# Optimization experiments

Hardware: AMD Instinct MI355X
Metric: run time of the kernel (lower is better)

The kernel has to match this reference:

```python
import jax, jax.numpy as jnp
import numpy as np

N_NODES = 100000
N_EDGES = 1600000


def _gcn_conv(x, src, dst, W, b, n_nodes):
    """PyG GCNConv: add self-loops, symmetric norm, linear, scatter-add."""
    h = x @ W  # [N, out]
    # append self-loops
    loop = jnp.arange(n_nodes, dtype=src.dtype)
    s = jnp.concatenate([src, loop])
    d = jnp.concatenate([dst, loop])
    # degree over destinations (with self-loops)
    deg = jax.ops.segment_sum(jnp.ones_like(d, dtype=h.dtype), d, num_segments=n_nodes)
    dinv = jax.lax.rsqrt(jnp.maximum(deg, 1.0))
    norm = dinv[s] * dinv[d]  # [E+N]
    msg = h[s] * norm[:, None]  # [E+N, out] gather + scale
    out = jax.ops.segment_sum(msg, d, num_segments=n_nodes)  # scatter-add
    return out + b


def setup_inputs() -> dict:
    key = jax.random.key(0)
    k1, k2, k3, k4 = jax.random.split(key, 4)
    x = jax.random.normal(k1, (N_NODES, 10), dtype=jnp.float32)
    edge_index = jax.random.randint(k2, (2, N_EDGES), 0, N_NODES, dtype=jnp.int64)
    W1 = jax.random.normal(k3, (10, 64), dtype=jnp.float32) * (1.0 / np.sqrt(10))
    b1 = jnp.zeros((64,), dtype=jnp.float32)
    W2 = jax.random.normal(k4, (64, 10), dtype=jnp.float32) * (1.0 / np.sqrt(64))
    b2 = jnp.zeros((10,), dtype=jnp.float32)
    return {"x": x, "edge_index": edge_index, "W1": W1, "b1": b1, "W2": W2, "b2": b2}


def reference(x, edge_index, W1, b1, W2, b2):
    src, dst = edge_index[0], edge_index[1]
    h = _gcn_conv(x, src, dst, W1, b1, N_NODES)
    h = jax.nn.relu(h)
    # dropout is identity in eval mode
    h = _gcn_conv(h, src, dst, W2, b2, N_NODES)
    return jax.nn.log_softmax(h, axis=1)
```

## Files before the change

### kernel.cpp

```cpp
#include <hip/hip_runtime.h>
#include <hip/hip_fp16.h>

#define N_NODES 100000
#define N_EDGES 1600000

#define NPB   256
#define NB    391
#define ABLK  256
#define ATHR  1024
#define BSLOT 64
#define CAP   64

typedef unsigned int u32;

__device__ __forceinline__ float2 h2f2(u32 u) {
    __half2 h = *reinterpret_cast<__half2*>(&u);
    return __half22float2(h);
}

__global__ __launch_bounds__(ATHR) void bucket_kernel(
    const int* __restrict__ src, const int* __restrict__ dst,
    int* __restrict__ gcnt, int* __restrict__ pairs, int E) {
    __shared__ int lcnt[NB];
    const int tid = threadIdx.x, blk = blockIdx.x;
    for (int b = tid; b < NB; b += ATHR) lcnt[b] = 0;
    __syncthreads();

    const int chunk = (E + gridDim.x - 1) / gridDim.x;
    const int e0 = blk * chunk;
    const int e1 = min(e0 + chunk, E);

    for (int e = e0 + tid; e < e1; e += ATHR) {
        int d = dst[e];
        int b = d >> 8;
        int p = (src[e] << 8) | (d & 255);
        int pos = atomicAdd(&lcnt[b], 1);
        if (pos < BSLOT) pairs[(size_t)b * (ABLK * BSLOT) + blk * BSLOT + pos] = p;
    }
    __syncthreads();
    for (int b = tid; b < NB; b += ATHR)
        gcnt[b * ABLK + blk] = min(lcnt[b], BSLOT);
}

__global__ __launch_bounds__(1024) void csr_kernel(
    const int* __restrict__ gcnt, const int* __restrict__ pairs,
    const float* __restrict__ x, int* __restrict__ cnt, int* __restrict__ slist,
    float* __restrict__ dinv, u32* __restrict__ xh, u32* __restrict__ th, int N) {
    __shared__ int ofs[NPB];
    __shared__ int gc[ABLK];
    const int b = blockIdx.x, tid = threadIdx.x;
    if (tid < NPB) ofs[tid] = 0;
    if (tid < ABLK) gc[tid] = gcnt[b * ABLK + tid];
    __syncthreads();
    const int* pb = pairs + (size_t)b * (ABLK * BSLOT);
    const int node0 = b * NPB;
    for (int i = tid; i < ABLK * BSLOT; i += 1024) {
        int r = i >> 6;
        int j = i & 63;
        if (j < gc[r]) {
            int p = pb[i];
            int dl = p & 255;
            int pos = atomicAdd(&ofs[dl], 1);
            if (pos < CAP) slist[(size_t)(node0 + dl) * CAP + pos] = p >> 8;
        }
    }
    __syncthreads();
    if (tid < NPB) {
        int node = node0 + tid;
        if (node < N) {
            int deg = min(ofs[tid], CAP);
            cnt[node] = deg;
            int padded = (deg + 3) & ~3;
            for (int j = deg; j < padded; ++j) slist[(size_t)node * CAP + j] = N_NODES;
            float di = rsqrtf((float)deg + 1.0f);
            dinv[node] = di;
            u32 h[8];
#pragma unroll
            for (int k = 0; k < 5; ++k) {
                __half2 hh = __floats2half2_rn(x[(size_t)node * 10 + 2 * k] * di,
                                               x[(size_t)node * 10 + 2 * k + 1] * di);
                h[k] = *reinterpret_cast<u32*>(&hh);
            }
            h[5] = h[6] = h[7] = 0u;
            u32* row = xh + (size_t)node * 8;
            ((uint4*)row)[0] = make_uint4(h[0], h[1], h[2], h[3]);
            ((uint4*)row)[1] = make_uint4(h[4], h[5], h[6], h[7]);
        }
    }
    if (b == 0 && tid == 0) {
        u32* rx = xh + (size_t)N * 8;
        u32* rt = th + (size_t)N * 8;
        ((uint4*)rx)[0] = make_uint4(0, 0, 0, 0); ((uint4*)rx)[1] = make_uint4(0, 0, 0, 0);
        ((uint4*)rt)[0] = make_uint4(0, 0, 0, 0); ((uint4*)rt)[1] = make_uint4(0, 0, 0, 0);
    }
}

__global__ void aggmlp_kernel(const u32* __restrict__ vh, const int* __restrict__ cnt,
                              const int* __restrict__ slist, const float* __restrict__ dinv,
                              const float* __restrict__ W1, const float* __restrict__ b1,
                              const float* __restrict__ W2, u32* __restrict__ th, int N) {
    __shared__ float sW1[640];
    __shared__ float sW2[640];
    __shared__ float sb1[64];
    for (int k = threadIdx.x; k < 640; k += blockDim.x) { sW1[k] = W1[k]; sW2[k] = W2[k]; }
    if (threadIdx.x < 64) sb1[threadIdx.x] = b1[threadIdx.x];
    __syncthreads();
    int gt = blockIdx.x * blockDim.x + threadIdx.x;
    int i = gt >> 1, cg = gt & 1;
    if (i >= N) return;
    int degi = cnt[i];
    const int* lst = slist + (size_t)i * CAP;
    float a[8];
    {
        uint4 s = *(((const uint4*)(vh + (size_t)i * 8)) + cg);
        float2 f0 = h2f2(s.x), f1 = h2f2(s.y), f2 = h2f2(s.z), f3 = h2f2(s.w);
        a[0] = f0.x; a[1] = f0.y; a[2] = f1.x; a[3] = f1.y;
        a[4] = f2.x; a[5] = f2.y; a[6] = f3.x; a[7] = f3.y;
    }
    for (int k = 0; k < degi; k += 4) {
        int4 s4 = *reinterpret_cast<const int4*>(lst + k);
        uint4 q0 = *(((const uint4*)(vh + (size_t)s4.x * 8)) + cg);
        uint4 q1 = *(((const uint4*)(vh + (size_t)s4.y * 8)) + cg);
        uint4 q2 = *(((const uint4*)(vh + (size_t)s4.z * 8)) + cg);
        uint4 q3 = *(((const uint4*)(vh + (size_t)s4.w * 8)) + cg);
        float2 f;
        f = h2f2(q0.x); a[0] += f.x; a[1] += f.y;  f = h2f2(q0.y); a[2] += f.x; a[3] += f.y;
        f = h2f2(q0.z); a[4] += f.x; a[5] += f.y;  f = h2f2(q0.w); a[6] += f.x; a[7] += f.y;
        f = h2f2(q1.x); a[0] += f.x; a[1] += f.y;  f = h2f2(q1.y); a[2] += f.x; a[3] += f.y;
        f = h2f2(q1.z); a[4] += f.x; a[5] += f.y;  f = h2f2(q1.w); a[6] += f.x; a[7] += f.y;
        f = h2f2(q2.x); a[0] += f.x; a[1] += f.y;  f = h2f2(q2.y); a[2] += f.x; a[3] += f.y;
        f = h2f2(q2.z); a[4] += f.x; a[5] += f.y;  f = h2f2(q2.w); a[6] += f.x; a[7] += f.y;
        f = h2f2(q3.x); a[0] += f.x; a[1] += f.y;  f = h2f2(q3.y); a[2] += f.x; a[3] += f.y;
        f = h2f2(q3.z); a[4] += f.x; a[5] += f.y;  f = h2f2(q3.w); a[6] += f.x; a[7] += f.y;
    }
    float t0 = __shfl_xor(a[0], 1), t1 = __shfl_xor(a[1], 1);
    float t2 = __shfl_xor(a[2], 1), t3 = __shfl_xor(a[3], 1);
    float t4 = __shfl_xor(a[4], 1), t5 = __shfl_xor(a[5], 1);
    float t6 = __shfl_xor(a[6], 1), t7 = __shfl_xor(a[7], 1);
    float di = dinv[i];
    float ax[10];
    if (cg == 0) {
        ax[0]=a[0]; ax[1]=a[1]; ax[2]=a[2]; ax[3]=a[3]; ax[4]=a[4];
        ax[5]=a[5]; ax[6]=a[6]; ax[7]=a[7]; ax[8]=t0;   ax[9]=t1;
    } else {
        ax[0]=t0; ax[1]=t1; ax[2]=t2; ax[3]=t3; ax[4]=t4;
        ax[5]=t5; ax[6]=t6; ax[7]=t7; ax[8]=a[0]; ax[9]=a[1];
    }
#pragma unroll
    for (int k = 0; k < 10; ++k) ax[k] *= di;
    float o[10];
#pragma unroll
    for (int k = 0; k < 10; ++k) o[k] = 0.f;
    const int c0 = cg * 32;
    for (int c = c0; c < c0 + 32; ++c) {
        float y = sb1[c];
#pragma unroll
        for (int k = 0; k < 10; ++k) y = fmaf(ax[k], sW1[k * 64 + c], y);
        y = fmaxf(y, 0.f);
#pragma unroll
        for (int k = 0; k < 10; ++k) o[k] = fmaf(y, sW2[c * 10 + k], o[k]);
    }
#pragma unroll
    for (int k = 0; k < 10; ++k) o[k] += __shfl_xor(o[k], 1);
#pragma unroll
    for (int k = 0; k < 10; ++k) o[k] *= di;
    u32* row = th + (size_t)i * 8;
    if (cg == 0) {
        __half2 h0 = __floats2half2_rn(o[0], o[1]);
        __half2 h1 = __floats2half2_rn(o[2], o[3]);
        __half2 h2 = __floats2half2_rn(o[4], o[5]);
        __half2 h3 = __floats2half2_rn(o[6], o[7]);
        ((uint4*)row)[0] = make_uint4(*reinterpret_cast<u32*>(&h0), *reinterpret_cast<u32*>(&h1),
                                      *reinterpret_cast<u32*>(&h2), *reinterpret_cast<u32*>(&h3));
    } else {
        __half2 h4 = __floats2half2_rn(o[8], o[9]);
        ((uint4*)row)[1] = make_uint4(*reinterpret_cast<u32*>(&h4), 0u, 0u, 0u);
    }
}

__global__ void aggout_kernel(const u32* __restrict__ vh, const int* __restrict__ cnt,
                              const int* __restrict__ slist, const float* __restrict__ dinv,
                              const float* __restrict__ b2, float* __restrict__ out, int N) {
    int gt = blockIdx.x * blockDim.x + threadIdx.x;
    int i = gt >> 1, cg = gt & 1;
    bool valid = (i < N);
    float a[8];
#pragma unroll
    for (int k = 0; k < 8; ++k) a[k] = 0.f;
    if (valid) {
        int degi = cnt[i];
        const int* lst = slist + (size_t)i * CAP;
        {
            uint4 s = *(((const uint4*)(vh + (size_t)i * 8)) + cg);
            float2 f0 = h2f2(s.x), f1 = h2f2(s.y), f2 = h2f2(s.z), f3 = h2f2(s.w);
            a[0] = f0.x; a[1] = f0.y; a[2] = f1.x; a[3] = f1.y;
            a[4] = f2.x; a[5] = f2.y; a[6] = f3.x; a[7] = f3.y;
        }
        for (int k = 0; k < degi; k += 4) {
            int4 s4 = *reinterpret_cast<const int4*>(lst + k);
            uint4 q0 = *(((const uint4*)(vh + (size_t)s4.x * 8)) + cg);
            uint4 q1 = *(((const uint4*)(vh + (size_t)s4.y * 8)) + cg);
            uint4 q2 = *(((const uint4*)(vh + (size_t)s4.z * 8)) + cg);
            uint4 q3 = *(((const uint4*)(vh + (size_t)s4.w * 8)) + cg);
            float2 f;
            f = h2f2(q0.x); a[0] += f.x; a[1] += f.y;  f = h2f2(q0.y); a[2] += f.x; a[3] += f.y;
            f = h2f2(q0.z); a[4] += f.x; a[5] += f.y;  f = h2f2(q0.w); a[6] += f.x; a[7] += f.y;
            f = h2f2(q1.x); a[0] += f.x; a[1] += f.y;  f = h2f2(q1.y); a[2] += f.x; a[3] += f.y;
            f = h2f2(q1.z); a[4] += f.x; a[5] += f.y;  f = h2f2(q1.w); a[6] += f.x; a[7] += f.y;
            f = h2f2(q2.x); a[0] += f.x; a[1] += f.y;  f = h2f2(q2.y); a[2] += f.x; a[3] += f.y;
            f = h2f2(q2.z); a[4] += f.x; a[5] += f.y;  f = h2f2(q2.w); a[6] += f.x; a[7] += f.y;
            f = h2f2(q3.x); a[0] += f.x; a[1] += f.y;  f = h2f2(q3.y); a[2] += f.x; a[3] += f.y;
            f = h2f2(q3.z); a[4] += f.x; a[5] += f.y;  f = h2f2(q3.w); a[6] += f.x; a[7] += f.y;
        }
    }
    float v8 = __shfl_xor(a[0], 1);
    float v9 = __shfl_xor(a[1], 1);
    if (valid && cg == 0) {
        float di = dinv[i];
        float v[10] = { a[0], a[1], a[2], a[3], a[4], a[5], a[6], a[7], v8, v9 };
        float m = -1e30f;
#pragma unroll
        for (int c = 0; c < 10; ++c) {
            v[c] = fmaf(di, v[c], b2[c]);
            m = fmaxf(m, v[c]);
        }
        float s = 0.f;
#pragma unroll
        for (int c = 0; c < 10; ++c) s += __expf(v[c] - m);
        float lse = __logf(s) + m;
        float2* po = (float2*)(out + (size_t)i * 10);
#pragma unroll
        for (int c = 0; c < 5; ++c) po[c] = make_float2(v[2 * c] - lse, v[2 * c + 1] - lse);
    }
}

extern "C" void kernel_launch(void* const* d_in, const int* in_sizes, int n_in,
                              void* d_out, int out_size, void* d_ws, size_t ws_size,
                              hipStream_t stream) {
    const float* x  = (const float*)d_in[0];
    const int*   ei = (const int*)d_in[1];
    const float* W1 = (const float*)d_in[2];
    const float* b1 = (const float*)d_in[3];
    const float* W2 = (const float*)d_in[4];
    const float* b2 = (const float*)d_in[5];
    float* out = (float*)d_out;

    const int N = N_NODES, E = N_EDGES;
    const int* src = ei;
    const int* dst = ei + E;

    int*   gcnt  = (int*)d_ws;
    int*   pairs = gcnt + (size_t)NB * ABLK;
    int*   cnt   = pairs + (size_t)NB * ABLK * BSLOT;
    int*   slist = cnt + N;
    float* dinv  = (float*)(slist + (size_t)N * CAP);
    u32*   xh    = (u32*)(dinv + N);
    u32*   th    = xh + (size_t)(N + 1) * 8;

    bucket_kernel<<<ABLK, ATHR, 0, stream>>>(src, dst, gcnt, pairs, E);
    csr_kernel<<<NB, 1024, 0, stream>>>(gcnt, pairs, x, cnt, slist, dinv, xh, th, N);
    aggmlp_kernel<<<(2 * N + 255) / 256, 256, 0, stream>>>(xh, cnt, slist, dinv, W1, b1, W2, th, N);
    aggout_kernel<<<(2 * N + 255) / 256, 256, 0, stream>>>(th, cnt, slist, dinv, b2, out, N);
}
```

Measured before the change: 83.17 us.

## Fuse the four GCN kernels into one persistent kernel with grid barriers

Merges bucketing, CSR build, layer-1 aggregation plus MLP, and layer-2 aggregation plus log-softmax into a single persistent kernel of 256 blocks of 1024 threads. The stages are separated by atomic spin-wait grid barriers, and a tiny init kernel resets the barrier counter. The aim is to remove the inter-kernel launch gaps and drain/fill between stages. In exchange the grid size and occupancy are fixed for every phase: 391 buckets are processed by 256 blocks, leaving some blocks with two. Correctness also depends on all blocks being co-resident.

New measurement: 174.3 us. 2.1x slower.

```diff
diff --git a/kernel.cpp b/kernel.cpp
--- a/kernel.cpp
+++ b/kernel.cpp
@@ -6,8 +6,8 @@
 
 #define NPB   256
 #define NB    391
-#define ABLK  256
-#define ATHR  1024
+#define GBLK  256
+#define GTHR  1024
 #define BSLOT 64
 #define CAP   64
 
@@ -18,219 +18,239 @@
     return __half22float2(h);
 }
 
-__global__ __launch_bounds__(ATHR) void bucket_kernel(
+__global__ void init_kernel(int* __restrict__ bar) {
+    if (threadIdx.x == 0) *bar = 0;
+}
+
+__device__ __forceinline__ void gridbar(int* bar, int target) {
+    __syncthreads();
+    if (threadIdx.x == 0) {
+        __threadfence();
+        atomicAdd(bar, 1);
+        while (__hip_atomic_load(bar, __ATOMIC_RELAXED, __HIP_MEMORY_SCOPE_AGENT) < target) {
+            __builtin_amdgcn_s_sleep(1);
+        }
+        __threadfence();
+    }
+    __syncthreads();
+}
+
+__global__ __launch_bounds__(GTHR) void mega_kernel(
     const int* __restrict__ src, const int* __restrict__ dst,
-    int* __restrict__ gcnt, int* __restrict__ pairs, int E) {
-    __shared__ int lcnt[NB];
-    const int tid = threadIdx.x, blk = blockIdx.x;
-    for (int b = tid; b < NB; b += ATHR) lcnt[b] = 0;
-    __syncthreads();
-
-    const int chunk = (E + gridDim.x - 1) / gridDim.x;
-    const int e0 = blk * chunk;
-    const int e1 = min(e0 + chunk, E);
-
-    for (int e = e0 + tid; e < e1; e += ATHR) {
-        int d = dst[e];
-        int b = d >> 8;
-        int p = (src[e] << 8) | (d & 255);
-        int pos = atomicAdd(&lcnt[b], 1);
-        if (pos < BSLOT) pairs[(size_t)b * (ABLK * BSLOT) + blk * BSLOT + pos] = p;
-    }
-    __syncthreads();
-    for (int b = tid; b < NB; b += ATHR)
-        gcnt[b * ABLK + blk] = min(lcnt[b], BSLOT);
-}
-
-__global__ __launch_bounds__(1024) void csr_kernel(
-    const int* __restrict__ gcnt, const int* __restrict__ pairs,
-    const float* __restrict__ x, int* __restrict__ cnt, int* __restrict__ slist,
-    float* __restrict__ dinv, u32* __restrict__ xh, u32* __restrict__ th, int N) {
-    __shared__ int ofs[NPB];
-    __shared__ int gc[ABLK];
-    const int b = blockIdx.x, tid = threadIdx.x;
-    if (tid < NPB) ofs[tid] = 0;
-    if (tid < ABLK) gc[tid] = gcnt[b * ABLK + tid];
-    __syncthreads();
-    const int* pb = pairs + (size_t)b * (ABLK * BSLOT);
-    const int node0 = b * NPB;
-    for (int i = tid; i < ABLK * BSLOT; i += 1024) {
-        int r = i >> 6;
-        int j = i & 63;
-        if (j < gc[r]) {
-            int p = pb[i];
-            int dl = p & 255;
-            int pos = atomicAdd(&ofs[dl], 1);
-            if (pos < CAP) slist[(size_t)(node0 + dl) * CAP + pos] = p >> 8;
-        }
-    }
-    __syncthreads();
-    if (tid < NPB) {
-        int node = node0 + tid;
-        if (node < N) {
-            int deg = min(ofs[tid], CAP);
-            cnt[node] = deg;
-            int padded = (deg + 3) & ~3;
-            for (int j = deg; j < padded; ++j) slist[(size_t)node * CAP + j] = N_NODES;
-            float di = rsqrtf((float)deg + 1.0f);
-            dinv[node] = di;
-            u32 h[8];
-#pragma unroll
-            for (int k = 0; k < 5; ++k) {
-                __half2 hh = __floats2half2_rn(x[(size_t)node * 10 + 2 * k] * di,
-                                               x[(size_t)node * 10 + 2 * k + 1] * di);
-                h[k] = *reinterpret_cast<u32*>(&hh);
-            }
-            h[5] = h[6] = h[7] = 0u;
-            u32* row = xh + (size_t)node * 8;
-            ((uint4*)row)[0] = make_uint4(h[0], h[1], h[2], h[3]);
-            ((uint4*)row)[1] = make_uint4(h[4], h[5], h[6], h[7]);
-        }
-    }
-    if (b == 0 && tid == 0) {
+    const float* __restrict__ x,
+    const float* __restrict__ W1, const float* __restrict__ b1,
+    const float* __restrict__ W2, const float* __restrict__ b2,
+    int* __restrict__ bar, int* __restrict__ gcnt, int* __restrict__ pairs,
+    int* __restrict__ cnt, int* __restrict__ slist, float* __restrict__ dinv,
+    u32* __restrict__ xh, u32* __restrict__ th, float* __restrict__ out,
+    int N, int E) {
+
+    __shared__ int   lcnt[NB];
+    __shared__ int   s_ofs[NPB];
+    __shared__ int   s_gc[GBLK];
+    __shared__ float sW1[640];
+    __shared__ float sW2[640];
+    __shared__ float sb1[64];
+
+    const int tid = threadIdx.x;
+    const int blk = blockIdx.x;
+
+    for (int b = tid; b < NB; b += GTHR) lcnt[b] = 0;
+    __syncthreads();
+    {
+        const int chunk = (E + GBLK - 1) / GBLK;
+        const int e0 = blk * chunk;
+        const int e1 = min(e0 + chunk, E);
+        for (int e = e0 + tid; e < e1; e += GTHR) {
+            int d = dst[e];
+            int b = d >> 8;
+            int p = (src[e] << 8) | (d & 255);
+            int pos = atomicAdd(&lcnt[b], 1);
+            if (pos < BSLOT) pairs[(size_t)b * (GBLK * BSLOT) + blk * BSLOT + pos] = p;
+        }
+        __syncthreads();
+        for (int b = tid; b < NB; b += GTHR)
+            gcnt[b * GBLK + blk] = min(lcnt[b], BSLOT);
+    }
+    gridbar(bar, GBLK);
+
+    for (int b = blk; b < NB; b += GBLK) {
+        if (tid < NPB) s_ofs[tid] = 0;
+        if (tid < GBLK) s_gc[tid] = gcnt[b * GBLK + tid];
+        __syncthreads();
+        const int* pb = pairs + (size_t)b * (GBLK * BSLOT);
+        const int node0 = b * NPB;
+        for (int i = tid; i < GBLK * BSLOT; i += GTHR) {
+            int r = i >> 6;
+            int j = i & 63;
+            if (j < s_gc[r]) {
+                int p = pb[i];
+                int dl = p & 255;
+                int pos = atomicAdd(&s_ofs[dl], 1);
+                if (pos < CAP) slist[(size_t)(node0 + dl) * CAP + pos] = p >> 8;
+            }
+        }
+        __syncthreads();
+        if (tid < NPB) {
+            int node = node0 + tid;
+            if (node < N) {
+                int deg = min(s_ofs[tid], CAP);
+                cnt[node] = deg;
+                int padded = (deg + 3) & ~3;
+                for (int j = deg; j < padded; ++j) slist[(size_t)node * CAP + j] = N_NODES;
+                float di = rsqrtf((float)deg + 1.0f);
+                dinv[node] = di;
+                u32 h[8];
+#pragma unroll
+                for (int k = 0; k < 5; ++k) {
+                    __half2 hh = __floats2half2_rn(x[(size_t)node * 10 + 2 * k] * di,
+                                                   x[(size_t)node * 10 + 2 * k + 1] * di);
+                    h[k] = *reinterpret_cast<u32*>(&hh);
+                }
+                h[5] = h[6] = h[7] = 0u;
+                u32* row = xh + (size_t)node * 8;
+                ((uint4*)row)[0] = make_uint4(h[0], h[1], h[2], h[3]);
+                ((uint4*)row)[1] = make_uint4(h[4], h[5], h[6], h[7]);
+            }
+        }
+        __syncthreads();
+    }
+    if (blk == 0 && tid == 0) {
         u32* rx = xh + (size_t)N * 8;
         u32* rt = th + (size_t)N * 8;
         ((uint4*)rx)[0] = make_uint4(0, 0, 0, 0); ((uint4*)rx)[1] = make_uint4(0, 0, 0, 0);
         ((uint4*)rt)[0] = make_uint4(0, 0, 0, 0); ((uint4*)rt)[1] = make_uint4(0, 0, 0, 0);
     }
-}
-
-__global__ void aggmlp_kernel(const u32* __restrict__ vh, const int* __restrict__ cnt,
-                              const int* __restrict__ slist, const float* __restrict__ dinv,
-                              const float* __restrict__ W1, const float* __restrict__ b1,
-                              const float* __restrict__ W2, u32* __restrict__ th, int N) {
-    __shared__ float sW1[640];
-    __shared__ float sW2[640];
-    __shared__ float sb1[64];
-    for (int k = threadIdx.x; k < 640; k += blockDim.x) { sW1[k] = W1[k]; sW2[k] = W2[k]; }
-    if (threadIdx.x < 64) sb1[threadIdx.x] = b1[threadIdx.x];
-    __syncthreads();
-    int gt = blockIdx.x * blockDim.x + threadIdx.x;
-    int i = gt >> 1, cg = gt & 1;
-    if (i >= N) return;
-    int degi = cnt[i];
-    const int* lst = slist + (size_t)i * CAP;
-    float a[8];
+    gridbar(bar, 2 * GBLK);
+
+    for (int k = tid; k < 640; k += GTHR) { sW1[k] = W1[k]; sW2[k] = W2[k]; }
+    if (tid < 64) sb1[tid] = b1[tid];
+    __syncthreads();
     {
-        uint4 s = *(((const uint4*)(vh + (size_t)i * 8)) + cg);
-        float2 f0 = h2f2(s.x), f1 = h2f2(s.y), f2 = h2f2(s.z), f3 = h2f2(s.w);
-        a[0] = f0.x; a[1] = f0.y; a[2] = f1.x; a[3] = f1.y;
-        a[4] = f2.x; a[5] = f2.y; a[6] = f3.x; a[7] = f3.y;
-    }
-    for (int k = 0; k < degi; k += 4) {
-        int4 s4 = *reinterpret_cast<const int4*>(lst + k);
-        uint4 q0 = *(((const uint4*)(vh + (size_t)s4.x * 8)) + cg);
-        uint4 q1 = *(((const uint4*)(vh + (size_t)s4.y * 8)) + cg);
-        uint4 q2 = *(((const uint4*)(vh + (size_t)s4.z * 8)) + cg);
-        uint4 q3 = *(((const uint4*)(vh + (size_t)s4.w * 8)) + cg);
-        float2 f;
-        f = h2f2(q0.x); a[0] += f.x; a[1] += f.y;  f = h2f2(q0.y); a[2] += f.x; a[3] += f.y;
-        f = h2f2(q0.z); a[4] += f.x; a[5] += f.y;  f = h2f2(q0.w); a[6] += f.x; a[7] += f.y;
-        f = h2f2(q1.x); a[0] += f.x; a[1] += f.y;  f = h2f2(q1.y); a[2] += f.x; a[3] += f.y;
-        f = h2f2(q1.z); a[4] += f.x; a[5] += f.y;  f = h2f2(q1.w); a[6] += f.x; a[7] += f.y;
-        f = h2f2(q2.x); a[0] += f.x; a[1] += f.y;  f = h2f2(q2.y); a[2] += f.x; a[3] += f.y;
-        f = h2f2(q2.z); a[4] += f.x; a[5] += f.y;  f = h2f2(q2.w); a[6] += f.x; a[7] += f.y;
-        f = h2f2(q3.x); a[0] += f.x; a[1] += f.y;  f = h2f2(q3.y); a[2] += f.x; a[3] += f.y;
-        f = h2f2(q3.z); a[4] += f.x; a[5] += f.y;  f = h2f2(q3.w); a[6] += f.x; a[7] += f.y;
-    }
-    float t0 = __shfl_xor(a[0], 1), t1 = __shfl_xor(a[1], 1);
-    float t2 = __shfl_xor(a[2], 1), t3 = __shfl_xor(a[3], 1);
-    float t4 = __shfl_xor(a[4], 1), t5 = __shfl_xor(a[5], 1);
-    float t6 = __shfl_xor(a[6], 1), t7 = __shfl_xor(a[7], 1);
-    float di = dinv[i];
-    float ax[10];
-    if (cg == 0) {
-        ax[0]=a[0]; ax[1]=a[1]; ax[2]=a[2]; ax[3]=a[3]; ax[4]=a[4];
-        ax[5]=a[5]; ax[6]=a[6]; ax[7]=a[7]; ax[8]=t0;   ax[9]=t1;
-    } else {
-        ax[0]=t0; ax[1]=t1; ax[2]=t2; ax[3]=t3; ax[4]=t4;
-        ax[5]=t5; ax[6]=t6; ax[7]=t7; ax[8]=a[0]; ax[9]=a[1];
-    }
-#pragma unroll
-    for (int k = 0; k < 10; ++k) ax[k] *= di;
-    float o[10];
-#pragma unroll
-    for (int k = 0; k < 10; ++k) o[k] = 0.f;
-    const int c0 = cg * 32;
-    for (int c = c0; c < c0 + 32; ++c) {
-        float y = sb1[c];
-#pragma unroll
-        for (int k = 0; k < 10; ++k) y = fmaf(ax[k], sW1[k * 64 + c], y);
-        y = fmaxf(y, 0.f);
-#pragma unroll
-        for (int k = 0; k < 10; ++k) o[k] = fmaf(y, sW2[c * 10 + k], o[k]);
-    }
-#pragma unroll
-    for (int k = 0; k < 10; ++k) o[k] += __shfl_xor(o[k], 1);
-#pragma unroll
-    for (int k = 0; k < 10; ++k) o[k] *= di;
-    u32* row = th + (size_t)i * 8;
-    if (cg == 0) {
-        __half2 h0 = __floats2half2_rn(o[0], o[1]);
-        __half2 h1 = __floats2half2_rn(o[2], o[3]);
-        __half2 h2 = __floats2half2_rn(o[4], o[5]);
-        __half2 h3 = __floats2half2_rn(o[6], o[7]);
-        ((uint4*)row)[0] = make_uint4(*reinterpret_cast<u32*>(&h0), *reinterpret_cast<u32*>(&h1),
-                                      *reinterpret_cast<u32*>(&h2), *reinterpret_cast<u32*>(&h3));
-    } else {
-        __half2 h4 = __floats2half2_rn(o[8], o[9]);
-        ((uint4*)row)[1] = make_uint4(*reinterpret_cast<u32*>(&h4), 0u, 0u, 0u);
-    }
-}
-
-__global__ void aggout_kernel(const u32* __restrict__ vh, const int* __restrict__ cnt,
-                              const int* __restrict__ slist, const float* __restrict__ dinv,
-                              const float* __restrict__ b2, float* __restrict__ out, int N) {
-    int gt = blockIdx.x * blockDim.x + threadIdx.x;
-    int i = gt >> 1, cg = gt & 1;
-    bool valid = (i < N);
-    float a[8];
-#pragma unroll
-    for (int k = 0; k < 8; ++k) a[k] = 0.f;
-    if (valid) {
-        int degi = cnt[i];
-        const int* lst = slist + (size_t)i * CAP;
-        {
-            uint4 s = *(((const uint4*)(vh + (size_t)i * 8)) + cg);
-            float2 f0 = h2f2(s.x), f1 = h2f2(s.y), f2 = h2f2(s.z), f3 = h2f2(s.w);
-            a[0] = f0.x; a[1] = f0.y; a[2] = f1.x; a[3] = f1.y;
-            a[4] = f2.x; a[5] = f2.y; a[6] = f3.x; a[7] = f3.y;
-        }
-        for (int k = 0; k < degi; k += 4) {
-            int4 s4 = *reinterpret_cast<const int4*>(lst + k);
-            uint4 q0 = *(((const uint4*)(vh + (size_t)s4.x * 8)) + cg);
-            uint4 q1 = *(((const uint4*)(vh + (size_t)s4.y * 8)) + cg);
-            uint4 q2 = *(((const uint4*)(vh + (size_t)s4.z * 8)) + cg);
-            uint4 q3 = *(((const uint4*)(vh + (size_t)s4.w * 8)) + cg);
-            float2 f;
-            f = h2f2(q0.x); a[0] += f.x; a[1] += f.y;  f = h2f2(q0.y); a[2] += f.x; a[3] += f.y;
-            f = h2f2(q0.z); a[4] += f.x; a[5] += f.y;  f = h2f2(q0.w); a[6] += f.x; a[7] += f.y;
-            f = h2f2(q1.x); a[0] += f.x; a[1] += f.y;  f = h2f2(q1.y); a[2] += f.x; a[3] += f.y;
-            f = h2f2(q1.z); a[4] += f.x; a[5] += f.y;  f = h2f2(q1.w); a[6] += f.x; a[7] += f.y;
-            f = h2f2(q2.x); a[0] += f.x; a[1] += f.y;  f = h2f2(q2.y); a[2] += f.x; a[3] += f.y;
-            f = h2f2(q2.z); a[4] += f.x; a[5] += f.y;  f = h2f2(q2.w); a[6] += f.x; a[7] += f.y;
-            f = h2f2(q3.x); a[0] += f.x; a[1] += f.y;  f = h2f2(q3.y); a[2] += f.x; a[3] += f.y;
-            f = h2f2(q3.z); a[4] += f.x; a[5] += f.y;  f = h2f2(q3.w); a[6] += f.x; a[7] += f.y;
-        }
-    }
-    float v8 = __shfl_xor(a[0], 1);
-    float v9 = __shfl_xor(a[1], 1);
-    if (valid && cg == 0) {
-        float di = dinv[i];
-        float v[10] = { a[0], a[1], a[2], a[3], a[4], a[5], a[6], a[7], v8, v9 };
-        float m = -1e30f;
-#pragma unroll
-        for (int c = 0; c < 10; ++c) {
-            v[c] = fmaf(di, v[c], b2[c]);
-            m = fmaxf(m, v[c]);
-        }
-        float s = 0.f;
-#pragma unroll
-        for (int c = 0; c < 10; ++c) s += __expf(v[c] - m);
-        float lse = __logf(s) + m;
-        float2* po = (float2*)(out + (size_t)i * 10);
-#pragma unroll
-        for (int c = 0; c < 5; ++c) po[c] = make_float2(v[2 * c] - lse, v[2 * c + 1] - lse);
+        int gt = blk * GTHR + tid;
+        int i = gt >> 1, cg = gt & 1;
+        if (i < N) {
+            int degi = cnt[i];
+            const int* lst = slist + (size_t)i * CAP;
+            float a[8];
+            {
+                uint4 s = *(((const uint4*)(xh + (size_t)i * 8)) + cg);
+                float2 f0 = h2f2(s.x), f1 = h2f2(s.y), f2 = h2f2(s.z), f3 = h2f2(s.w);
+                a[0] = f0.x; a[1] = f0.y; a[2] = f1.x; a[3] = f1.y;
+                a[4] = f2.x; a[5] = f2.y; a[6] = f3.x; a[7] = f3.y;
+            }
+            for (int k = 0; k < degi; k += 4) {
+                int4 s4 = *reinterpret_cast<const int4*>(lst + k);
+                uint4 q0 = *(((const uint4*)(xh + (size_t)s4.x * 8)) + cg);
+                uint4 q1 = *(((const uint4*)(xh + (size_t)s4.y * 8)) + cg);
+                uint4 q2 = *(((const uint4*)(xh + (size_t)s4.z * 8)) + cg);
+                uint4 q3 = *(((const uint4*)(xh + (size_t)s4.w * 8)) + cg);
+                float2 f;
+                f = h2f2(q0.x); a[0] += f.x; a[1] += f.y;  f = h2f2(q0.y); a[2] += f.x; a[3] += f.y;
+                f = h2f2(q0.z); a[4] += f.x; a[5] += f.y;  f = h2f2(q0.w); a[6] += f.x; a[7] += f.y;
+                f = h2f2(q1.x); a[0] += f.x; a[1] += f.y;  f = h2f2(q1.y); a[2] += f.x; a[3] += f.y;
+                f = h2f2(q1.z); a[4] += f.x; a[5] += f.y;  f = h2f2(q1.w); a[6] += f.x; a[7] += f.y;
+                f = h2f2(q2.x); a[0] += f.x; a[1] += f.y;  f = h2f2(q2.y); a[2] += f.x; a[3] += f.y;
+                f = h2f2(q2.z); a[4] += f.x; a[5] += f.y;  f = h2f2(q2.w); a[6] += f.x; a[7] += f.y;
+                f = h2f2(q3.x); a[0] += f.x; a[1] += f.y;  f = h2f2(q3.y); a[2] += f.x; a[3] += f.y;
+                f = h2f2(q3.z); a[4] += f.x; a[5] += f.y;  f = h2f2(q3.w); a[6] += f.x; a[7] += f.y;
+            }
+            float t0 = __shfl_xor(a[0], 1), t1 = __shfl_xor(a[1], 1);
+            float t2 = __shfl_xor(a[2], 1), t3 = __shfl_xor(a[3], 1);
+            float t4 = __shfl_xor(a[4], 1), t5 = __shfl_xor(a[5], 1);
+            float t6 = __shfl_xor(a[6], 1), t7 = __shfl_xor(a[7], 1);
+            float di = dinv[i];
+            float ax[10];
+            if (cg == 0) {
+                ax[0]=a[0]; ax[1]=a[1]; ax[2]=a[2]; ax[3]=a[3]; ax[4]=a[4];
+                ax[5]=a[5]; ax[6]=a[6]; ax[7]=a[7]; ax[8]=t0;   ax[9]=t1;
+            } else {
+                ax[0]=t0; ax[1]=t1; ax[2]=t2; ax[3]=t3; ax[4]=t4;
+                ax[5]=t5; ax[6]=t6; ax[7]=t7; ax[8]=a[0]; ax[9]=a[1];
+            }
+#pragma unroll
+            for (int k = 0; k < 10; ++k) ax[k] *= di;
+            float o[10];
+#pragma unroll
+            for (int k = 0; k < 10; ++k) o[k] = 0.f;
+            const int c0 = cg * 32;
+            for (int c = c0; c < c0 + 32; ++c) {
+                float y = sb1[c];
+#pragma unroll
+                for (int k = 0; k < 10; ++k) y = fmaf(ax[k], sW1[k * 64 + c], y);
+                y = fmaxf(y, 0.f);
+#pragma unroll
+                for (int k = 0; k < 10; ++k) o[k] = fmaf(y, sW2[c * 10 + k], o[k]);
+            }
+#pragma unroll
+            for (int k = 0; k < 10; ++k) o[k] += __shfl_xor(o[k], 1);
+#pragma unroll
+            for (int k = 0; k < 10; ++k) o[k] *= di;
+            u32* row = th + (size_t)i * 8;
+            if (cg == 0) {
+                __half2 h0 = __floats2half2_rn(o[0], o[1]);
+                __half2 h1 = __floats2half2_rn(o[2], o[3]);
+                __half2 h2 = __floats2half2_rn(o[4], o[5]);
+                __half2 h3 = __floats2half2_rn(o[6], o[7]);
+                ((uint4*)row)[0] = make_uint4(*reinterpret_cast<u32*>(&h0), *reinterpret_cast<u32*>(&h1),
+                                              *reinterpret_cast<u32*>(&h2), *reinterpret_cast<u32*>(&h3));
+            } else {
+                __half2 h4 = __floats2half2_rn(o[8], o[9]);
+                ((uint4*)row)[1] = make_uint4(*reinterpret_cast<u32*>(&h4), 0u, 0u, 0u);
+            }
+        }
+    }
+    gridbar(bar, 3 * GBLK);
+
+    {
+        int gt = blk * GTHR + tid;
+        int i = gt >> 1, cg = gt & 1;
+        if (i < N) {
+            int degi = cnt[i];
+            const int* lst = slist + (size_t)i * CAP;
+            float a[8];
+            {
+                uint4 s = *(((const uint4*)(th + (size_t)i * 8)) + cg);
+                float2 f0 = h2f2(s.x), f1 = h2f2(s.y), f2 = h2f2(s.z), f3 = h2f2(s.w);
+                a[0] = f0.x; a[1] = f0.y; a[2] = f1.x; a[3] = f1.y;
+                a[4] = f2.x; a[5] = f2.y; a[6] = f3.x; a[7] = f3.y;
+            }
+            for (int k = 0; k < degi; k += 4) {
+                int4 s4 = *reinterpret_cast<const int4*>(lst + k);
+                uint4 q0 = *(((const uint4*)(th + (size_t)s4.x * 8)) + cg);
+                uint4 q1 = *(((const uint4*)(th + (size_t)s4.y * 8)) + cg);
+                uint4 q2 = *(((const uint4*)(th + (size_t)s4.z * 8)) + cg);
+                uint4 q3 = *(((const uint4*)(th + (size_t)s4.w * 8)) + cg);
+                float2 f;
+                f = h2f2(q0.x); a[0] += f.x; a[1] += f.y;  f = h2f2(q0.y); a[2] += f.x; a[3] += f.y;
+                f = h2f2(q0.z); a[4] += f.x; a[5] += f.y;  f = h2f2(q0.w); a[6] += f.x; a[7] += f.y;
+                f = h2f2(q1.x); a[0] += f.x; a[1] += f.y;  f = h2f2(q1.y); a[2] += f.x; a[3] += f.y;
+                f = h2f2(q1.z); a[4] += f.x; a[5] += f.y;  f = h2f2(q1.w); a[6] += f.x; a[7] += f.y;
+                f = h2f2(q2.x); a[0] += f.x; a[1] += f.y;  f = h2f2(q2.y); a[2] += f.x; a[3] += f.y;
+                f = h2f2(q2.z); a[4] += f.x; a[5] += f.y;  f = h2f2(q2.w); a[6] += f.x; a[7] += f.y;
+                f = h2f2(q3.x); a[0] += f.x; a[1] += f.y;  f = h2f2(q3.y); a[2] += f.x; a[3] += f.y;
+                f = h2f2(q3.z); a[4] += f.x; a[5] += f.y;  f = h2f2(q3.w); a[6] += f.x; a[7] += f.y;
+            }
+            float v8 = __shfl_xor(a[0], 1);
+            float v9 = __shfl_xor(a[1], 1);
+            if (cg == 0) {
+                float di = dinv[i];
+                float v[10] = { a[0], a[1], a[2], a[3], a[4], a[5], a[6], a[7], v8, v9 };
+                float m = -1e30f;
+#pragma unroll
+                for (int c = 0; c < 10; ++c) {
+                    v[c] = fmaf(di, v[c], b2[c]);
+                    m = fmaxf(m, v[c]);
+                }
+                float s = 0.f;
+#pragma unroll
+                for (int c = 0; c < 10; ++c) s += __expf(v[c] - m);
+                float lse = __logf(s) + m;
+                float2* po = (float2*)(out + (size_t)i * 10);
+#pragma unroll
+                for (int c = 0; c < 5; ++c) po[c] = make_float2(v[2 * c] - lse, v[2 * c + 1] - lse);
+            }
+        }
     }
 }
 
@@ -249,16 +269,17 @@
     const int* src = ei;
     const int* dst = ei + E;
 
-    int*   gcnt  = (int*)d_ws;
-    int*   pairs = gcnt + (size_t)NB * ABLK;
-    int*   cnt   = pairs + (size_t)NB * ABLK * BSLOT;
+    int*   bar   = (int*)d_ws;
+    int*   gcnt  = bar + 512;
+    int*   pairs = gcnt + (size_t)NB * GBLK;
+    int*   cnt   = pairs + (size_t)NB * GBLK * BSLOT;
     int*   slist = cnt + N;
     float* dinv  = (float*)(slist + (size_t)N * CAP);
     u32*   xh    = (u32*)(dinv + N);
     u32*   th    = xh + (size_t)(N + 1) * 8;
 
-    bucket_kernel<<<ABLK, ATHR, 0, stream>>>(src, dst, gcnt, pairs, E);
-    csr_kernel<<<NB, 1024, 0, stream>>>(gcnt, pairs, x, cnt, slist, dinv, xh, th, N);
-    aggmlp_kernel<<<(2 * N + 255) / 256, 256, 0, stream>>>(xh, cnt, slist, dinv, W1, b1, W2, th, N);
-    aggout_kernel<<<(2 * N + 255) / 256, 256, 0, stream>>>(th, cnt, slist, dinv, b2, out, N);
-}
+    init_kernel<<<1, 64, 0, stream>>>(bar);
+    mega_kernel<<<GBLK, GTHR, 0, stream>>>(src, dst, x, W1, b1, W2, b2,
+                                           bar, gcnt, pairs, cnt, slist, dinv,
+                                           xh, th, out, N, E);
+}
```
